# Performance work log

Measured on AMD Instinct MI355X. Metric: run time of the kernel, lower is better.

## Reference

```python
import jax, jax.numpy as jnp
import numpy as np

SOS = 4998
EOS = 4999
SCALING = 2.0


def setup_inputs() -> dict:
    key = jax.random.key(0)
    ks = jax.random.split(key, 12)
    B, T, E, D, A, C, F, ODIM, L = 32, 1000, 512, 1024, 512, 10, 100, 5000, 100
    s = 0.02
    return {
        "hpad": jax.random.normal(ks[0], (B, T, E), jnp.float32),
        "ys": jax.random.randint(ks[1], (B, L), 0, SOS, jnp.int32),
        # AttLoc params
        "w_enc": jax.random.normal(ks[2], (A, E), jnp.float32) * s,
        "b_enc": jnp.zeros((A,), jnp.float32),
        "w_dec": jax.random.normal(ks[3], (A, D), jnp.float32) * s,
        "w_att": jax.random.normal(ks[4], (A, C), jnp.float32) * s,
        "w_conv": jax.random.normal(ks[5], (C, 1, 2 * F + 1), jnp.float32) * s,  # OIH 1D conv kernel
        "w_gvec": jax.random.normal(ks[6], (1, A), jnp.float32) * s,
        "b_gvec": jnp.zeros((1,), jnp.float32),
        # Decoder params
        "embed": jax.random.normal(ks[7], (ODIM, D), jnp.float32) * s,
        "w_ih": jax.random.normal(ks[8], (4 * D, D + E), jnp.float32) * s,
        "w_hh": jax.random.normal(ks[9], (4 * D, D), jnp.float32) * s,
        "b_ih": jnp.zeros((4 * D,), jnp.float32),
        "b_hh": jnp.zeros((4 * D,), jnp.float32),
        "w_out": jax.random.normal(ks[10], (ODIM, D), jnp.float32) * s,
        "b_out": jnp.zeros((ODIM,), jnp.float32),
    }


def _decode(hpad, ys, w_enc, b_enc, w_dec, w_att, w_conv, w_gvec, b_gvec,
            embed, w_ih, w_hh, b_ih, b_hh, w_out, b_out):
    B, T, E = hpad.shape
    D = w_hh.shape[1]
    F = (w_conv.shape[-1] - 1) // 2
    # ys_in = [sos; y] per utterance (all same length -> already padded)
    ys_in = jnp.concatenate([jnp.full((B, 1), SOS, ys.dtype), ys], axis=1)  # [B, olen]
    eys = embed[ys_in]                                                      # [B, olen, D]
    # pre_compute_enc_h = mlp_enc(enc_h)
    pre = jnp.einsum('bte,ae->bta', hpad, w_enc) + b_enc                    # [B, T, A]
    att0 = jnp.full((B, T), 1.0 / T, hpad.dtype)   # uniform init attention (all hlen == T)
    z0 = jnp.zeros((B, D), hpad.dtype)
    c0 = jnp.zeros((B, D), hpad.dtype)

    def step(carry, ey_i):
        z, c, aw = carry
        # location-aware conv over previous attention weights: [B,1,T] -> [B,C,T]
        conv = jax.lax.conv_general_dilated(aw[:, None, :], w_conv, (1,), [(F, F)],
                                            dimension_numbers=('NCH', 'OIH', 'NCH'))
        att_feat = jnp.einsum('bct,ac->bta', conv, w_att)                   # mlp_att
        dec = (z @ w_dec.T)[:, None, :]                                     # mlp_dec, tiled
        e = jnp.tanh(att_feat + pre + dec) @ w_gvec[0] + b_gvec[0]          # [B, T]
        w = jax.nn.softmax(SCALING * e, axis=1)
        ctx = jnp.einsum('bt,bte->be', w, hpad)                             # [B, E]
        # LSTMCell
        x = jnp.concatenate([ey_i, ctx], axis=1)                            # [B, D+E]
        gates = x @ w_ih.T + b_ih + z @ w_hh.T + b_hh
        i_g, f_g, g_g, o_g = jnp.split(gates, 4, axis=1)
        c_new = jax.nn.sigmoid(f_g) * c + jax.nn.sigmoid(i_g) * jnp.tanh(g_g)
        z_new = jax.nn.sigmoid(o_g) * jnp.tanh(c_new)
        return (z_new, c_new, w), z_new

    _, z_all = jax.lax.scan(step, (z0, c0, att0), jnp.swapaxes(eys, 0, 1))  # [olen, B, D]
    y_all = jnp.einsum('obd,vd->obv', z_all, w_out) + b_out                 # [olen, B, odim]
    return jnp.swapaxes(y_all, 0, 1)                                        # [B, olen, odim]


def reference(hpad, ys, w_enc, b_enc, w_dec, w_att, w_conv, w_gvec, b_gvec,
              embed, w_ih, w_hh, b_ih, b_hh, w_out, b_out):
    return _decode(hpad, ys, w_enc, b_enc, w_dec, w_att, w_conv, w_gvec, b_gvec,
                   embed, w_ih, w_hh, b_ih, b_hh, w_out, b_out)
```

## Files before the change

### kernel.cpp

```cpp
#include <hip/hip_runtime.h>
#include <math.h>

#define B_    32
#define T_    1000
#define E_    512
#define D_    1024
#define A_    512
#define C_    10
#define F_    100
#define ODIM_ 5000
#define OLEN_ 101
#define SOS_  4998

#define OFF_PRE   0u
#define N_PRE     (32u*1000u*512u)
#define OFF_DEC   (OFF_PRE + N_PRE)
#define N_DEC     (32u*512u)
#define OFF_CONV  (OFF_DEC + N_DEC)
#define N_CONVB   (32u*10u*1000u)
#define OFF_EB    (OFF_CONV + N_CONVB)
#define N_EB      (32u*1000u)
#define OFF_AW    (OFF_EB + N_EB)
#define OFF_CTX   (OFF_AW + N_EB)
#define N_CTX     (32u*512u)
#define OFF_GP    (OFF_CTX + N_CTX)
#define N_GP      (10u*32u*4096u)
#define OFF_Z     (OFF_GP + N_GP)
#define N_Z       (32u*1024u)
#define OFF_C     (OFF_Z + N_Z)
#define OFF_ZALL  (OFF_C + N_Z)

__device__ __forceinline__ float fast_tanh(float x) {
    float cx = fminf(8.f, fmaxf(-8.f, x));
    float e = __expf(2.f * cx);
    return (e - 1.f) * __builtin_amdgcn_rcpf(e + 1.f);
}
__device__ __forceinline__ float fast_sigmoid(float x) {
    float cx = fminf(30.f, fmaxf(-30.f, x));
    return __builtin_amdgcn_rcpf(1.f + __expf(-cx));
}

__global__ __launch_bounds__(256) void k_init(float* ws) {
    int i = blockIdx.x * 256 + threadIdx.x;
    if (i < (int)N_Z) { ws[OFF_Z + i] = 0.f; ws[OFF_C + i] = 0.f; }
    if (i < (int)N_EB) ws[OFF_AW + i] = 1.0f / (float)T_;
}

__global__ __launch_bounds__(256) void k_pre(const float* __restrict__ hp,
                                             const float* __restrict__ we,
                                             const float* __restrict__ be,
                                             float* __restrict__ pre) {
    __shared__ float As[64][68];
    __shared__ float Bs[64][68];
    int m0 = blockIdx.y * 64, n0 = blockIdx.x * 64;
    int tid = threadIdx.x;
    int tr = tid >> 4, tc = tid & 15;
    float acc[4][4] = {};
    for (int k0 = 0; k0 < 512; k0 += 64) {
        for (int i = tid; i < 1024; i += 256) {
            int m = i >> 4, kq = (i & 15) << 2;
            float4 v = *(const float4*)&hp[(size_t)(m0 + m) * 512 + k0 + kq];
            As[kq + 0][m] = v.x; As[kq + 1][m] = v.y; As[kq + 2][m] = v.z; As[kq + 3][m] = v.w;
            float4 w = *(const float4*)&we[(size_t)(n0 + m) * 512 + k0 + kq];
            Bs[kq + 0][m] = w.x; Bs[kq + 1][m] = w.y; Bs[kq + 2][m] = w.z; Bs[kq + 3][m] = w.w;
        }
        __syncthreads();
        #pragma unroll 16
        for (int kk = 0; kk < 64; ++kk) {
            float4 av = *(const float4*)&As[kk][tr << 2];
            float4 bv = *(const float4*)&Bs[kk][tc << 2];
            float a[4] = {av.x, av.y, av.z, av.w};
            float b[4] = {bv.x, bv.y, bv.z, bv.w};
            #pragma unroll
            for (int i = 0; i < 4; i++)
                #pragma unroll
                for (int j = 0; j < 4; j++) acc[i][j] += a[i] * b[j];
        }
        __syncthreads();
    }
    #pragma unroll
    for (int i = 0; i < 4; i++) {
        int m = m0 + (tr << 2) + i;
        int n = n0 + (tc << 2);
        float4 o;
        o.x = acc[i][0] + be[n + 0];
        o.y = acc[i][1] + be[n + 1];
        o.z = acc[i][2] + be[n + 2];
        o.w = acc[i][3] + be[n + 3];
        *(float4*)&pre[(size_t)m * 512 + n] = o;
    }
}

__global__ __launch_bounds__(256) void k_prep(const float* __restrict__ wdec,
                                              const float* __restrict__ wconv,
                                              float* ws) {
    int tid = threadIdx.x;
    if (blockIdx.x < 1024) {
        int gw = blockIdx.x * 4 + (tid >> 6);
        int lane = tid & 63;
        int b = gw >> 9, a = gw & 511;
        const float4* wr = (const float4*)(wdec + (size_t)a * 1024);
        const float4* zr = (const float4*)(ws + OFF_Z + b * 1024);
        float acc = 0.f;
        #pragma unroll
        for (int i = 0; i < 4; i++) {
            float4 w4 = wr[i * 64 + lane];
            float4 z4 = zr[i * 64 + lane];
            acc += w4.x * z4.x + w4.y * z4.y + w4.z * z4.z + w4.w * z4.w;
        }
        #pragma unroll
        for (int off = 32; off > 0; off >>= 1) acc += __shfl_xor(acc, off, 64);
        if (lane == 0) ws[OFF_DEC + b * 512 + a] = acc;
    } else {
        int blk = blockIdx.x - 1024;
        int b = blk / 10, c = blk - b * 10;
        if (tid >= 250) return;
        int t = tid * 4;
        const float* ar = ws + OFF_AW + b * 1000;
        const float* wc = wconv + c * 201;
        float a0, a1, a2, a3;
        a0 = (t - 100 >= 0) ? ar[t - 100] : 0.f;
        a1 = (t -  99 >= 0) ? ar[t -  99] : 0.f;
        a2 = (t -  98 >= 0) ? ar[t -  98] : 0.f;
        a3 = (t -  97 >= 0) ? ar[t -  97] : 0.f;
        float c0 = 0.f, c1 = 0.f, c2 = 0.f, c3 = 0.f;
        #pragma unroll 4
        for (int j = 0; j < 201; ++j) {
            float w = wc[j];
            c0 += a0 * w; c1 += a1 * w; c2 += a2 * w; c3 += a3 * w;
            a0 = a1; a1 = a2; a2 = a3;
            int ni = t + j - 96;
            a3 = (ni >= 0 && ni < 1000) ? ar[ni] : 0.f;
        }
        float* o = ws + OFF_CONV + (size_t)(b * 10 + c) * 1000 + t;
        o[0] = c0; o[1] = c1; o[2] = c2; o[3] = c3;
    }
}

__global__ __launch_bounds__(64) void k_energy(const float* __restrict__ watt,
                                               const float* __restrict__ gvec,
                                               const float* __restrict__ bg,
                                               float* ws) {
    int b  = blockIdx.x / 50;
    int t0 = (blockIdx.x - b * 50) * 20;
    int lane = threadIdx.x;
    int a0 = lane * 4, a1 = 256 + lane * 4;
    float wr[8][10];
    #pragma unroll
    for (int i = 0; i < 4; i++)
        #pragma unroll
        for (int c = 0; c < 10; c++) {
            wr[i][c]     = watt[(a0 + i) * 10 + c];
            wr[4 + i][c] = watt[(a1 + i) * 10 + c];
        }
    float4 d0 = *(const float4*)&ws[OFF_DEC + b * 512 + a0];
    float4 d1 = *(const float4*)&ws[OFF_DEC + b * 512 + a1];
    float4 g0 = *(const float4*)&gvec[a0];
    float4 g1 = *(const float4*)&gvec[a1];
    float dc[8] = {d0.x, d0.y, d0.z, d0.w, d1.x, d1.y, d1.z, d1.w};
    float gv[8] = {g0.x, g0.y, g0.z, g0.w, g1.x, g1.y, g1.z, g1.w};
    float bgv = bg[0];
    const float* convb = ws + OFF_CONV + b * 10000;
    for (int it = 0; it < 20; ++it) {
        int t = t0 + it;
        const float* pr = ws + OFF_PRE + (size_t)(b * 1000 + t) * 512;
        float4 p0 = *(const float4*)&pr[a0];
        float4 p1 = *(const float4*)&pr[a1];
        float cv[10];
        #pragma unroll
        for (int c = 0; c < 10; c++) cv[c] = convb[c * 1000 + t];
        float pa[8] = {p0.x, p0.y, p0.z, p0.w, p1.x, p1.y, p1.z, p1.w};
        float acc = 0.f;
        #pragma unroll
        for (int i = 0; i < 8; i++) {
            float s = pa[i] + dc[i];
            #pragma unroll
            for (int c = 0; c < 10; c++) s += cv[c] * wr[i][c];
            acc += gv[i] * fast_tanh(s);
        }
        #pragma unroll
        for (int off = 32; off > 0; off >>= 1) acc += __shfl_xor(acc, off, 64);
        if (lane == 0) ws[OFF_EB + b * 1000 + t] = acc + bgv;
    }
}

__global__ __launch_bounds__(256) void k_softmax(float* ws) {
    int b = blockIdx.x, tid = threadIdx.x;
    ws[OFF_CTX + b * 512 + tid] = 0.f;
    ws[OFF_CTX + b * 512 + 256 + tid] = 0.f;
    __shared__ float red[256];
    const float* e = ws + OFF_EB + b * 1000;
    float s[4];
    float m = -1e30f;
    #pragma unroll
    for (int j = 0; j < 4; j++) {
        int t = tid + j * 256;
        s[j] = (t < 1000) ? 2.0f * e[t] : -1e30f;
        m = fmaxf(m, s[j]);
    }
    red[tid] = m; __syncthreads();
    for (int off = 128; off > 0; off >>= 1) {
        if (tid < off) red[tid] = fmaxf(red[tid], red[tid + off]);
        __syncthreads();
    }
    m = red[0]; __syncthreads();
    float p[4], sum = 0.f;
    #pragma unroll
    for (int j = 0; j < 4; j++) {
        int t = tid + j * 256;
        p[j] = (t < 1000) ? __expf(s[j] - m) : 0.f;
        sum += p[j];
    }
    red[tid] = sum; __syncthreads();
    for (int off = 128; off > 0; off >>= 1) {
        if (tid < off) red[tid] += red[tid + off];
        __syncthreads();
    }
    float inv = __builtin_amdgcn_rcpf(red[0]);
    #pragma unroll
    for (int j = 0; j < 4; j++) {
        int t = tid + j * 256;
        if (t < 1000) ws[OFF_AW + b * 1000 + t] = p[j] * inv;
    }
}

__global__ __launch_bounds__(128) void k_ctx(const float* __restrict__ hp, float* ws) {
    int b = blockIdx.x >> 5, ts = blockIdx.x & 31;
    int e4 = threadIdx.x;
    const float* awr = ws + OFF_AW + b * 1000;
    const float4* hp4 = (const float4*)hp;
    int t0 = ts * 32;
    int t1 = t0 + 32; if (t1 > 1000) t1 = 1000;
    float4 acc = make_float4(0.f, 0.f, 0.f, 0.f);
    for (int t = t0; t < t1; ++t) {
        float w = awr[t];
        float4 h = hp4[(size_t)(b * 1000 + t) * 128 + e4];
        acc.x += w * h.x; acc.y += w * h.y; acc.z += w * h.z; acc.w += w * h.w;
    }
    float* cx = ws + OFF_CTX + b * 512 + e4 * 4;
    atomicAdd(cx + 0, acc.x); atomicAdd(cx + 1, acc.y);
    atomicAdd(cx + 2, acc.z); atomicAdd(cx + 3, acc.w);
}

__global__ __launch_bounds__(128) void k_gates(const float* __restrict__ wih,
                                               const float* __restrict__ whh,
                                               const float* __restrict__ embed,
                                               const int* __restrict__ ys,
                                               float* ws, int step) {
    __shared__ float wlds[32][68];
    __shared__ float xs[32][36];
    int nt = blockIdx.x & 63;
    int ks = blockIdx.x >> 6;
    int n0 = nt * 64;
    int tid = threadIdx.x;
    int nq = tid & 15, bq = tid >> 4;
    float acc[4][4] = {};
    for (int kc = 0; kc < 8; ++kc) {
        int k0 = ks * 256 + kc * 32;
        {
            int r = tid >> 1, h = tid & 1;
            int gn = n0 + r;
            const float* wrow = (k0 < 1536)
                ? (wih + (size_t)gn * 1536 + k0 + h * 16)
                : (whh + (size_t)gn * 1024 + (k0 - 1536) + h * 16);
            #pragma unroll
            for (int j = 0; j < 4; ++j) {
                float4 v = *(const float4*)&wrow[j * 4];
                int kb = h * 16 + j * 4;
                wlds[kb + 0][r] = v.x; wlds[kb + 1][r] = v.y;
                wlds[kb + 2][r] = v.z; wlds[kb + 3][r] = v.w;
            }
        }
        {
            int b = tid >> 2, q = tid & 3;
            int tok = (step == 0) ? SOS_ : ys[b * 100 + step - 1];
            #pragma unroll
            for (int j = 0; j < 2; ++j) {
                int kk = k0 + q * 8 + j * 4;
                float4 v;
                if (kk < 1024)       v = *(const float4*)&embed[(size_t)tok * 1024 + kk];
                else if (kk < 1536)  v = *(const float4*)&ws[OFF_CTX + b * 512 + kk - 1024];
                else                 v = *(const float4*)&ws[OFF_Z + b * 1024 + kk - 1536];
                int kb = q * 8 + j * 4;
                xs[kb + 0][b] = v.x; xs[kb + 1][b] = v.y;
                xs[kb + 2][b] = v.z; xs[kb + 3][b] = v.w;
            }
        }
        __syncthreads();
        #pragma unroll 8
        for (int kk = 0; kk < 32; ++kk) {
            float4 wv = *(const float4*)&wlds[kk][nq * 4];
            float4 xv = *(const float4*)&xs[kk][bq * 4];
            float wa[4] = {wv.x, wv.y, wv.z, wv.w};
            float xa[4] = {xv.x, xv.y, xv.z, xv.w};
            #pragma unroll
            for (int i = 0; i < 4; i++)
                #pragma unroll
                for (int j = 0; j < 4; j++) acc[i][j] += wa[i] * xa[j];
        }
        __syncthreads();
    }
    float* gp = ws + OFF_GP + (size_t)(ks * 32 + bq * 4) * 4096 + n0 + nq * 4;
    #pragma unroll
    for (int j = 0; j < 4; j++)
        #pragma unroll
        for (int i = 0; i < 4; i++)
            gp[(size_t)j * 4096 + i] = acc[i][j];
}

__global__ __launch_bounds__(256) void k_lstm(const float* __restrict__ bih,
                                              const float* __restrict__ bhh,
                                              float* ws, int step) {
    int id = blockIdx.x * 256 + threadIdx.x;
    int b = id >> 10, d = id & 1023;
    float gi = bih[d] + bhh[d];
    float gf = bih[1024 + d] + bhh[1024 + d];
    float gg = bih[2048 + d] + bhh[2048 + d];
    float go = bih[3072 + d] + bhh[3072 + d];
    const float* gp = ws + OFF_GP;
    #pragma unroll
    for (int kc = 0; kc < 10; kc++) {
        const float* r = gp + (size_t)(kc * 32 + b) * 4096;
        gi += r[d];
        gf += r[1024 + d];
        gg += r[2048 + d];
        go += r[3072 + d];
    }
    float c_old = ws[OFF_C + id];
    float si = fast_sigmoid(gi);
    float sf = fast_sigmoid(gf);
    float so = fast_sigmoid(go);
    float cn = sf * c_old + si * fast_tanh(gg);
    float h = so * fast_tanh(cn);
    ws[OFF_C + id] = cn;
    ws[OFF_Z + id] = h;
    ws[OFF_ZALL + ((size_t)step * 32 + b) * 1024 + d] = h;
}

__global__ __launch_bounds__(256) void k_out(const float* __restrict__ zall,
                                             const float* __restrict__ wo,
                                             const float* __restrict__ bo,
                                             float* __restrict__ out) {
    __shared__ float As[64][68];
    __shared__ float Bs[64][68];
    int m0 = blockIdx.y * 64, n0 = blockIdx.x * 64;
    int tid = threadIdx.x;
    int tr = tid >> 4, tc = tid & 15;
    float acc[4][4] = {};
    for (int k0 = 0; k0 < 1024; k0 += 64) {
        for (int i = tid; i < 1024; i += 256) {
            int m = i >> 4, kq = (i & 15) << 2;
            int gm = m0 + m;
            float4 v = (gm < 3232) ? *(const float4*)&zall[(size_t)gm * 1024 + k0 + kq]
                                   : make_float4(0.f, 0.f, 0.f, 0.f);
            As[kq + 0][m] = v.x; As[kq + 1][m] = v.y; As[kq + 2][m] = v.z; As[kq + 3][m] = v.w;
            int gn = n0 + m;
            float4 w = (gn < 5000) ? *(const float4*)&wo[(size_t)gn * 1024 + k0 + kq]
                                   : make_float4(0.f, 0.f, 0.f, 0.f);
            Bs[kq + 0][m] = w.x; Bs[kq + 1][m] = w.y; Bs[kq + 2][m] = w.z; Bs[kq + 3][m] = w.w;
        }
        __syncthreads();
        #pragma unroll 16
        for (int kk = 0; kk < 64; ++kk) {
            float4 av = *(const float4*)&As[kk][tr << 2];
            float4 bv = *(const float4*)&Bs[kk][tc << 2];
            float a[4] = {av.x, av.y, av.z, av.w};
            float b[4] = {bv.x, bv.y, bv.z, bv.w};
            #pragma unroll
            for (int i = 0; i < 4; i++)
                #pragma unroll
                for (int j = 0; j < 4; j++) acc[i][j] += a[i] * b[j];
        }
        __syncthreads();
    }
    #pragma unroll
    for (int i = 0; i < 4; i++) {
        int m = m0 + (tr << 2) + i;
        if (m >= 3232) continue;
        int b = m & 31, o = m >> 5;
        #pragma unroll
        for (int j = 0; j < 4; j++) {
            int v = n0 + (tc << 2) + j;
            if (v < 5000)
                out[((size_t)b * 101 + o) * 5000 + v] = acc[i][j] + bo[v];
        }
    }
}

extern "C" void kernel_launch(void* const* d_in, const int* in_sizes, int n_in,
                              void* d_out, int out_size, void* d_ws, size_t ws_size,
                              hipStream_t stream) {
    const float* hpad   = (const float*)d_in[0];
    const int*   ys     = (const int*)d_in[1];
    const float* w_enc  = (const float*)d_in[2];
    const float* b_enc  = (const float*)d_in[3];
    const float* w_dec  = (const float*)d_in[4];
    const float* w_att  = (const float*)d_in[5];
    const float* w_conv = (const float*)d_in[6];
    const float* w_gvec = (const float*)d_in[7];
    const float* b_gvec = (const float*)d_in[8];
    const float* embed  = (const float*)d_in[9];
    const float* w_ih   = (const float*)d_in[10];
    const float* w_hh   = (const float*)d_in[11];
    const float* b_ih   = (const float*)d_in[12];
    const float* b_hh   = (const float*)d_in[13];
    const float* w_out  = (const float*)d_in[14];
    const float* b_out  = (const float*)d_in[15];
    float* ws  = (float*)d_ws;
    float* out = (float*)d_out;

    k_init<<<128, 256, 0, stream>>>(ws);
    k_pre<<<dim3(8, 500), 256, 0, stream>>>(hpad, w_enc, b_enc, ws + OFF_PRE);

    for (int step = 0; step < OLEN_; ++step) {
        k_prep<<<1024 + 320, 256, 0, stream>>>(w_dec, w_conv, ws);
        k_energy<<<1600, 64, 0, stream>>>(w_att, w_gvec, b_gvec, ws);
        k_softmax<<<32, 256, 0, stream>>>(ws);
        k_ctx<<<1024, 128, 0, stream>>>(hpad, ws);
        k_gates<<<640, 128, 0, stream>>>(w_ih, w_hh, embed, ys, ws, step);
        k_lstm<<<128, 256, 0, stream>>>(b_ih, b_hh, ws, step);
    }

    k_out<<<dim3(79, 51), 256, 0, stream>>>(ws + OFF_ZALL, w_out, b_out, out);
}
```

Before: 10.90 ms.

## Restructure decoder step into four kernels with split-softmax and fused gates/LSTM

Reduces the per-step kernel chain from six launches to four. The gate GEMM parts that do not depend on the attention context (embedding and recurrent terms) move into the first prep kernel. The energy kernel now emits per-chunk softmax max/sum partials, so the context kernel finalizes the softmax itself and the separate softmax launch goes away. The context part of the gates GEMM is fused with the split-K reduction and the LSTM cell update. The decoder projection also reuses each loaded w_dec row across four batch rows. The aim is to cut launch and serialization overhead in the sequential loop, at the cost of redundant max/sum recomputation in every ctx block and a small 128-block final kernel.

```diff
diff --git a/kernel.cpp b/kernel.cpp
--- a/kernel.cpp
+++ b/kernel.cpp
@@ -21,10 +21,13 @@
 #define OFF_EB    (OFF_CONV + N_CONVB)
 #define N_EB      (32u*1000u)
 #define OFF_AW    (OFF_EB + N_EB)
-#define OFF_CTX   (OFF_AW + N_EB)
+#define OFF_MS    (OFF_AW + N_EB)
+#define N_MS      (32u*100u)
+#define OFF_SS    (OFF_MS + N_MS)
+#define OFF_CTX   (OFF_SS + N_MS)
 #define N_CTX     (32u*512u)
 #define OFF_GP    (OFF_CTX + N_CTX)
-#define N_GP      (10u*32u*4096u)
+#define N_GP      (8u*32u*4096u)
 #define OFF_Z     (OFF_GP + N_GP)
 #define N_Z       (32u*1024u)
 #define OFF_C     (OFF_Z + N_Z)
@@ -43,6 +46,7 @@
 __global__ __launch_bounds__(256) void k_init(float* ws) {
     int i = blockIdx.x * 256 + threadIdx.x;
     if (i < (int)N_Z) { ws[OFF_Z + i] = 0.f; ws[OFF_C + i] = 0.f; }
+    if (i < (int)N_CTX) ws[OFF_CTX + i] = 0.f;
     if (i < (int)N_EB) ws[OFF_AW + i] = 1.0f / (float)T_;
 }
 
@@ -91,27 +95,62 @@
     }
 }
 
-__global__ __launch_bounds__(256) void k_prep(const float* __restrict__ wdec,
-                                              const float* __restrict__ wconv,
-                                              float* ws) {
+__global__ __launch_bounds__(256) void k_prepA(const float* __restrict__ wdec,
+                                               const float* __restrict__ wconv,
+                                               const float* __restrict__ wih,
+                                               const float* __restrict__ whh,
+                                               const float* __restrict__ embed,
+                                               const int* __restrict__ ys,
+                                               float* ws, int step) {
     int tid = threadIdx.x;
     if (blockIdx.x < 1024) {
-        int gw = blockIdx.x * 4 + (tid >> 6);
+        if (blockIdx.x < 64) ws[OFF_CTX + blockIdx.x * 256 + tid] = 0.f;
+        int w = blockIdx.x * 4 + (tid >> 6);
         int lane = tid & 63;
-        int b = gw >> 9, a = gw & 511;
+        int a = w >> 3, bg = w & 7;
         const float4* wr = (const float4*)(wdec + (size_t)a * 1024);
-        const float4* zr = (const float4*)(ws + OFF_Z + b * 1024);
-        float acc = 0.f;
-        #pragma unroll
-        for (int i = 0; i < 4; i++) {
-            float4 w4 = wr[i * 64 + lane];
-            float4 z4 = zr[i * 64 + lane];
-            acc += w4.x * z4.x + w4.y * z4.y + w4.z * z4.z + w4.w * z4.w;
-        }
-        #pragma unroll
-        for (int off = 32; off > 0; off >>= 1) acc += __shfl_xor(acc, off, 64);
-        if (lane == 0) ws[OFF_DEC + b * 512 + a] = acc;
-    } else {
+        float4 w4[4];
+        #pragma unroll
+        for (int i = 0; i < 4; i++) w4[i] = wr[i * 64 + lane];
+        float acc0 = 0.f, acc1 = 0.f, acc2 = 0.f, acc3 = 0.f;
+        {
+            const float4* zr = (const float4*)(ws + OFF_Z + (bg * 4 + 0) * 1024);
+            #pragma unroll
+            for (int i = 0; i < 4; i++) { float4 z4 = zr[i * 64 + lane];
+                acc0 += w4[i].x*z4.x + w4[i].y*z4.y + w4[i].z*z4.z + w4[i].w*z4.w; }
+        }
+        {
+            const float4* zr = (const float4*)(ws + OFF_Z + (bg * 4 + 1) * 1024);
+            #pragma unroll
+            for (int i = 0; i < 4; i++) { float4 z4 = zr[i * 64 + lane];
+                acc1 += w4[i].x*z4.x + w4[i].y*z4.y + w4[i].z*z4.z + w4[i].w*z4.w; }
+        }
+        {
+            const float4* zr = (const float4*)(ws + OFF_Z + (bg * 4 + 2) * 1024);
+            #pragma unroll
+            for (int i = 0; i < 4; i++) { float4 z4 = zr[i * 64 + lane];
+                acc2 += w4[i].x*z4.x + w4[i].y*z4.y + w4[i].z*z4.z + w4[i].w*z4.w; }
+        }
+        {
+            const float4* zr = (const float4*)(ws + OFF_Z + (bg * 4 + 3) * 1024);
+            #pragma unroll
+            for (int i = 0; i < 4; i++) { float4 z4 = zr[i * 64 + lane];
+                acc3 += w4[i].x*z4.x + w4[i].y*z4.y + w4[i].z*z4.z + w4[i].w*z4.w; }
+        }
+        #pragma unroll
+        for (int off = 32; off > 0; off >>= 1) {
+            acc0 += __shfl_xor(acc0, off, 64);
+            acc1 += __shfl_xor(acc1, off, 64);
+            acc2 += __shfl_xor(acc2, off, 64);
+            acc3 += __shfl_xor(acc3, off, 64);
+        }
+        if (lane == 0) {
+            ws[OFF_DEC + (bg * 4 + 0) * 512 + a] = acc0;
+            ws[OFF_DEC + (bg * 4 + 1) * 512 + a] = acc1;
+            ws[OFF_DEC + (bg * 4 + 2) * 512 + a] = acc2;
+            ws[OFF_DEC + (bg * 4 + 3) * 512 + a] = acc3;
+        }
+    } else if (blockIdx.x < 1344) {
         int blk = blockIdx.x - 1024;
         int b = blk / 10, c = blk - b * 10;
         if (tid >= 250) return;
@@ -134,16 +173,71 @@
         }
         float* o = ws + OFF_CONV + (size_t)(b * 10 + c) * 1000 + t;
         o[0] = c0; o[1] = c1; o[2] = c2; o[3] = c3;
-    }
-}
-
-__global__ __launch_bounds__(64) void k_energy(const float* __restrict__ watt,
-                                               const float* __restrict__ gvec,
-                                               const float* __restrict__ bg,
-                                               float* ws) {
-    int b  = blockIdx.x / 50;
-    int t0 = (blockIdx.x - b * 50) * 20;
-    int lane = threadIdx.x;
+    } else {
+        __shared__ float wlds[32][132];
+        __shared__ float xs[32][36];
+        int blk = blockIdx.x - 1344;
+        int nt = blk & 31, ks = blk >> 5;
+        int n0 = nt * 128;
+        bool isE = (ks < 4);
+        int kloc = isE ? ks * 256 : (ks - 4) * 256;
+        int r = tid >> 1, h = tid & 1;
+        int bx = tid >> 3, q8 = tid & 7;
+        int tok = (step == 0) ? SOS_ : ys[bx * 100 + step - 1];
+        const float* xsrc = isE ? (embed + (size_t)tok * 1024 + kloc)
+                                : (ws + OFF_Z + (size_t)bx * 1024 + kloc);
+        int nq = tid & 31, bq = tid >> 5;
+        float acc[4][4] = {};
+        for (int kc = 0; kc < 8; ++kc) {
+            int koff = kc * 32;
+            {
+                const float* wrow = isE ? (wih + (size_t)(n0 + r) * 1536 + kloc + koff + h * 16)
+                                        : (whh + (size_t)(n0 + r) * 1024 + kloc + koff + h * 16);
+                #pragma unroll
+                for (int j = 0; j < 4; ++j) {
+                    float4 v = *(const float4*)&wrow[j * 4];
+                    int kb = h * 16 + j * 4;
+                    wlds[kb + 0][r] = v.x; wlds[kb + 1][r] = v.y;
+                    wlds[kb + 2][r] = v.z; wlds[kb + 3][r] = v.w;
+                }
+            }
+            {
+                float4 v = *(const float4*)&xsrc[koff + q8 * 4];
+                xs[q8 * 4 + 0][bx] = v.x; xs[q8 * 4 + 1][bx] = v.y;
+                xs[q8 * 4 + 2][bx] = v.z; xs[q8 * 4 + 3][bx] = v.w;
+            }
+            __syncthreads();
+            #pragma unroll 8
+            for (int kk = 0; kk < 32; ++kk) {
+                float4 wv = *(const float4*)&wlds[kk][nq * 4];
+                float4 xv = *(const float4*)&xs[kk][bq * 4];
+                float wa[4] = {wv.x, wv.y, wv.z, wv.w};
+                float xa[4] = {xv.x, xv.y, xv.z, xv.w};
+                #pragma unroll
+                for (int i = 0; i < 4; i++)
+                    #pragma unroll
+                    for (int j = 0; j < 4; j++) acc[i][j] += wa[i] * xa[j];
+            }
+            __syncthreads();
+        }
+        float* gp = ws + OFF_GP + (size_t)(ks * 32 + bq * 4) * 4096 + n0 + nq * 4;
+        #pragma unroll
+        for (int j = 0; j < 4; j++)
+            #pragma unroll
+            for (int i = 0; i < 4; i++)
+                gp[(size_t)j * 4096 + i] = acc[i][j];
+    }
+}
+
+__global__ __launch_bounds__(256) void k_energy2(const float* __restrict__ watt,
+                                                 const float* __restrict__ gvec,
+                                                 const float* __restrict__ bg,
+                                                 float* ws) {
+    int w = blockIdx.x * 4 + (threadIdx.x >> 6);
+    int lane = threadIdx.x & 63;
+    int b = w / 100;
+    int ch = w - b * 100;
+    int t0 = ch * 10;
     int a0 = lane * 4, a1 = 256 + lane * 4;
     float wr[8][10];
     #pragma unroll
@@ -161,7 +255,8 @@
     float gv[8] = {g0.x, g0.y, g0.z, g0.w, g1.x, g1.y, g1.z, g1.w};
     float bgv = bg[0];
     const float* convb = ws + OFF_CONV + b * 10000;
-    for (int it = 0; it < 20; ++it) {
+    float M = -1e30f, S = 0.f;
+    for (int it = 0; it < 10; ++it) {
         int t = t0 + it;
         const float* pr = ws + OFF_PRE + (size_t)(b * 1000 + t) * 512;
         float4 p0 = *(const float4*)&pr[a0];
@@ -180,161 +275,140 @@
         }
         #pragma unroll
         for (int off = 32; off > 0; off >>= 1) acc += __shfl_xor(acc, off, 64);
-        if (lane == 0) ws[OFF_EB + b * 1000 + t] = acc + bgv;
-    }
-}
-
-__global__ __launch_bounds__(256) void k_softmax(float* ws) {
-    int b = blockIdx.x, tid = threadIdx.x;
-    ws[OFF_CTX + b * 512 + tid] = 0.f;
-    ws[OFF_CTX + b * 512 + 256 + tid] = 0.f;
-    __shared__ float red[256];
-    const float* e = ws + OFF_EB + b * 1000;
-    float s[4];
-    float m = -1e30f;
-    #pragma unroll
-    for (int j = 0; j < 4; j++) {
-        int t = tid + j * 256;
-        s[j] = (t < 1000) ? 2.0f * e[t] : -1e30f;
-        m = fmaxf(m, s[j]);
-    }
-    red[tid] = m; __syncthreads();
-    for (int off = 128; off > 0; off >>= 1) {
-        if (tid < off) red[tid] = fmaxf(red[tid], red[tid + off]);
-        __syncthreads();
-    }
-    m = red[0]; __syncthreads();
-    float p[4], sum = 0.f;
-    #pragma unroll
-    for (int j = 0; j < 4; j++) {
-        int t = tid + j * 256;
-        p[j] = (t < 1000) ? __expf(s[j] - m) : 0.f;
-        sum += p[j];
-    }
-    red[tid] = sum; __syncthreads();
-    for (int off = 128; off > 0; off >>= 1) {
-        if (tid < off) red[tid] += red[tid + off];
-        __syncthreads();
-    }
-    float inv = __builtin_amdgcn_rcpf(red[0]);
-    #pragma unroll
-    for (int j = 0; j < 4; j++) {
-        int t = tid + j * 256;
-        if (t < 1000) ws[OFF_AW + b * 1000 + t] = p[j] * inv;
-    }
-}
-
-__global__ __launch_bounds__(128) void k_ctx(const float* __restrict__ hp, float* ws) {
+        float st = 2.f * (acc + bgv);
+        if (lane == 0) ws[OFF_EB + b * 1000 + t] = st;
+        float Mn = fmaxf(M, st);
+        S = S * __expf(M - Mn) + __expf(st - Mn);
+        M = Mn;
+    }
+    if (lane == 0) {
+        ws[OFF_MS + b * 100 + ch] = M;
+        ws[OFF_SS + b * 100 + ch] = S;
+    }
+}
+
+__global__ __launch_bounds__(128) void k_ctx2(const float* __restrict__ hp, float* ws) {
+    __shared__ float sm[100], ssum[100], wsh[32];
     int b = blockIdx.x >> 5, ts = blockIdx.x & 31;
-    int e4 = threadIdx.x;
-    const float* awr = ws + OFF_AW + b * 1000;
+    int tid = threadIdx.x;
+    if (tid < 100) {
+        sm[tid]   = ws[OFF_MS + b * 100 + tid];
+        ssum[tid] = ws[OFF_SS + b * 100 + tid];
+    }
+    __syncthreads();
+    float M = -1e30f;
+    for (int i = 0; i < 100; i++) M = fmaxf(M, sm[i]);
+    float S = 0.f;
+    for (int i = 0; i < 100; i++) S += ssum[i] * __expf(sm[i] - M);
+    float invS = __builtin_amdgcn_rcpf(S);
+    int t0 = ts * 32;
+    if (tid < 32) {
+        int t = t0 + tid;
+        float wv = 0.f;
+        if (t < 1000) {
+            wv = __expf(ws[OFF_EB + b * 1000 + t] - M) * invS;
+            ws[OFF_AW + b * 1000 + t] = wv;
+        }
+        wsh[tid] = wv;
+    }
+    __syncthreads();
+    int t1 = t0 + 32; if (t1 > 1000) t1 = 1000;
     const float4* hp4 = (const float4*)hp;
-    int t0 = ts * 32;
-    int t1 = t0 + 32; if (t1 > 1000) t1 = 1000;
     float4 acc = make_float4(0.f, 0.f, 0.f, 0.f);
     for (int t = t0; t < t1; ++t) {
-        float w = awr[t];
-        float4 h = hp4[(size_t)(b * 1000 + t) * 128 + e4];
-        acc.x += w * h.x; acc.y += w * h.y; acc.z += w * h.z; acc.w += w * h.w;
-    }
-    float* cx = ws + OFF_CTX + b * 512 + e4 * 4;
+        float wv = wsh[t - t0];
+        float4 h = hp4[(size_t)(b * 1000 + t) * 128 + tid];
+        acc.x += wv * h.x; acc.y += wv * h.y; acc.z += wv * h.z; acc.w += wv * h.w;
+    }
+    float* cx = ws + OFF_CTX + b * 512 + tid * 4;
     atomicAdd(cx + 0, acc.x); atomicAdd(cx + 1, acc.y);
     atomicAdd(cx + 2, acc.z); atomicAdd(cx + 3, acc.w);
 }
 
-__global__ __launch_bounds__(128) void k_gates(const float* __restrict__ wih,
-                                               const float* __restrict__ whh,
-                                               const float* __restrict__ embed,
-                                               const int* __restrict__ ys,
-                                               float* ws, int step) {
-    __shared__ float wlds[32][68];
+__global__ __launch_bounds__(128) void k_gl(const float* __restrict__ wih,
+                                            const float* __restrict__ bih,
+                                            const float* __restrict__ bhh,
+                                            float* ws, int step) {
+    __shared__ float wlds[32][36];
     __shared__ float xs[32][36];
-    int nt = blockIdx.x & 63;
-    int ks = blockIdx.x >> 6;
-    int n0 = nt * 64;
+    __shared__ float gl[32][33];
     int tid = threadIdx.x;
-    int nq = tid & 15, bq = tid >> 4;
-    float acc[4][4] = {};
-    for (int kc = 0; kc < 8; ++kc) {
-        int k0 = ks * 256 + kc * 32;
-        {
-            int r = tid >> 1, h = tid & 1;
-            int gn = n0 + r;
-            const float* wrow = (k0 < 1536)
-                ? (wih + (size_t)gn * 1536 + k0 + h * 16)
-                : (whh + (size_t)gn * 1024 + (k0 - 1536) + h * 16);
-            #pragma unroll
-            for (int j = 0; j < 4; ++j) {
-                float4 v = *(const float4*)&wrow[j * 4];
-                int kb = h * 16 + j * 4;
+    int d0 = blockIdx.x * 8;
+    int r = tid >> 2, h = tid & 3;
+    int ng_r = (r >> 3) * 1024 + d0 + (r & 7);
+    const float* wrow = wih + (size_t)ng_r * 1536 + 1024 + h * 8;
+    int bx = tid >> 2, q4 = tid & 3;
+    const float* xsrc = ws + OFF_CTX + (size_t)bx * 512 + q4 * 8;
+    int nq = tid & 7, bq = tid >> 3;
+    float acc[4][2] = {};
+    for (int kc = 0; kc < 16; ++kc) {
+        int k0 = kc * 32;
+        {
+            #pragma unroll
+            for (int j = 0; j < 2; ++j) {
+                float4 v = *(const float4*)&wrow[k0 + j * 4];
+                int kb = h * 8 + j * 4;
                 wlds[kb + 0][r] = v.x; wlds[kb + 1][r] = v.y;
                 wlds[kb + 2][r] = v.z; wlds[kb + 3][r] = v.w;
             }
         }
         {
-            int b = tid >> 2, q = tid & 3;
-            int tok = (step == 0) ? SOS_ : ys[b * 100 + step - 1];
             #pragma unroll
             for (int j = 0; j < 2; ++j) {
-                int kk = k0 + q * 8 + j * 4;
-                float4 v;
-                if (kk < 1024)       v = *(const float4*)&embed[(size_t)tok * 1024 + kk];
-                else if (kk < 1536)  v = *(const float4*)&ws[OFF_CTX + b * 512 + kk - 1024];
-                else                 v = *(const float4*)&ws[OFF_Z + b * 1024 + kk - 1536];
-                int kb = q * 8 + j * 4;
-                xs[kb + 0][b] = v.x; xs[kb + 1][b] = v.y;
-                xs[kb + 2][b] = v.z; xs[kb + 3][b] = v.w;
+                float4 v = *(const float4*)&xsrc[k0 + j * 4];
+                int kb = q4 * 8 + j * 4;
+                xs[kb + 0][bx] = v.x; xs[kb + 1][bx] = v.y;
+                xs[kb + 2][bx] = v.z; xs[kb + 3][bx] = v.w;
             }
         }
         __syncthreads();
         #pragma unroll 8
         for (int kk = 0; kk < 32; ++kk) {
             float4 wv = *(const float4*)&wlds[kk][nq * 4];
-            float4 xv = *(const float4*)&xs[kk][bq * 4];
-            float wa[4] = {wv.x, wv.y, wv.z, wv.w};
-            float xa[4] = {xv.x, xv.y, xv.z, xv.w};
-            #pragma unroll
-            for (int i = 0; i < 4; i++)
-                #pragma unroll
-                for (int j = 0; j < 4; j++) acc[i][j] += wa[i] * xa[j];
-        }
-        __syncthreads();
-    }
-    float* gp = ws + OFF_GP + (size_t)(ks * 32 + bq * 4) * 4096 + n0 + nq * 4;
+            float x0 = xs[kk][bq * 2 + 0];
+            float x1 = xs[kk][bq * 2 + 1];
+            acc[0][0] += wv.x * x0; acc[0][1] += wv.x * x1;
+            acc[1][0] += wv.y * x0; acc[1][1] += wv.y * x1;
+            acc[2][0] += wv.z * x0; acc[2][1] += wv.z * x1;
+            acc[3][0] += wv.w * x0; acc[3][1] += wv.w * x1;
+        }
+        __syncthreads();
+    }
     #pragma unroll
-    for (int j = 0; j < 4; j++)
-        #pragma unroll
-        for (int i = 0; i < 4; i++)
-            gp[(size_t)j * 4096 + i] = acc[i][j];
-}
-
-__global__ __launch_bounds__(256) void k_lstm(const float* __restrict__ bih,
-                                              const float* __restrict__ bhh,
-                                              float* ws, int step) {
-    int id = blockIdx.x * 256 + threadIdx.x;
-    int b = id >> 10, d = id & 1023;
-    float gi = bih[d] + bhh[d];
-    float gf = bih[1024 + d] + bhh[1024 + d];
-    float gg = bih[2048 + d] + bhh[2048 + d];
-    float go = bih[3072 + d] + bhh[3072 + d];
-    const float* gp = ws + OFF_GP;
+    for (int i = 0; i < 4; i++) {
+        int nl = nq * 4 + i;
+        int ng = (nl >> 3) * 1024 + d0 + (nl & 7);
+        float bb = bih[ng] + bhh[ng];
+        #pragma unroll
+        for (int j = 0; j < 2; j++) {
+            int b = bq * 2 + j;
+            float s = acc[i][j] + bb;
+            #pragma unroll
+            for (int sl = 0; sl < 8; sl++)
+                s += ws[OFF_GP + (size_t)(sl * 32 + b) * 4096 + ng];
+            gl[nl][b] = s;
+        }
+    }
+    __syncthreads();
     #pragma unroll
-    for (int kc = 0; kc < 10; kc++) {
-        const float* r = gp + (size_t)(kc * 32 + b) * 4096;
-        gi += r[d];
-        gf += r[1024 + d];
-        gg += r[2048 + d];
-        go += r[3072 + d];
-    }
-    float c_old = ws[OFF_C + id];
-    float si = fast_sigmoid(gi);
-    float sf = fast_sigmoid(gf);
-    float so = fast_sigmoid(go);
-    float cn = sf * c_old + si * fast_tanh(gg);
-    float h = so * fast_tanh(cn);
-    ws[OFF_C + id] = cn;
-    ws[OFF_Z + id] = h;
-    ws[OFF_ZALL + ((size_t)step * 32 + b) * 1024 + d] = h;
+    for (int u = 0; u < 2; u++) {
+        int o = tid * 2 + u;
+        int dl = o >> 5, b = o & 31;
+        float gi = gl[dl][b];
+        float gf = gl[8 + dl][b];
+        float gg = gl[16 + dl][b];
+        float go = gl[24 + dl][b];
+        int id = b * 1024 + d0 + dl;
+        float c_old = ws[OFF_C + id];
+        float si = fast_sigmoid(gi);
+        float sf = fast_sigmoid(gf);
+        float so = fast_sigmoid(go);
+        float cn = sf * c_old + si * fast_tanh(gg);
+        float hh = so * fast_tanh(cn);
+        ws[OFF_C + id] = cn;
+        ws[OFF_Z + id] = hh;
+        ws[OFF_ZALL + ((size_t)step * 32 + b) * 1024 + d0 + dl] = hh;
+    }
 }
 
 __global__ __launch_bounds__(256) void k_out(const float* __restrict__ zall,
@@ -413,12 +487,10 @@
     k_pre<<<dim3(8, 500), 256, 0, stream>>>(hpad, w_enc, b_enc, ws + OFF_PRE);
 
     for (int step = 0; step < OLEN_; ++step) {
-        k_prep<<<1024 + 320, 256, 0, stream>>>(w_dec, w_conv, ws);
-        k_energy<<<1600, 64, 0, stream>>>(w_att, w_gvec, b_gvec, ws);
-        k_softmax<<<32, 256, 0, stream>>>(ws);
-        k_ctx<<<1024, 128, 0, stream>>>(hpad, ws);
-        k_gates<<<640, 128, 0, stream>>>(w_ih, w_hh, embed, ys, ws, step);
-        k_lstm<<<128, 256, 0, stream>>>(b_ih, b_hh, ws, step);
+        k_prepA<<<1600, 256, 0, stream>>>(w_dec, w_conv, w_ih, w_hh, embed, ys, ws, step);
+        k_energy2<<<800, 256, 0, stream>>>(w_att, w_gvec, b_gvec, ws);
+        k_ctx2<<<1024, 128, 0, stream>>>(hpad, ws);
+        k_gl<<<128, 128, 0, stream>>>(w_ih, b_ih, b_hh, ws, step);
     }
 
     k_out<<<dim3(79, 51), 256, 0, stream>>>(ws + OFF_ZALL, w_out, b_out, out);
```

Measured after the change: 11.00 ms. Within noise of the previous version (+1.0%).
